# Optimization experiments

Hardware: AMD Instinct MI355X
Metric: run time of the kernel (lower is better)

The kernel has to match this reference:

```python
import jax, jax.numpy as jnp
import numpy as np

B, T = 128, 64
N_IN, H1, H2, N_OUT = 2048, 2048, 1024, 128
BETA = 0.95
THRESH = 1.0  # snn.Leaky default threshold


def spike(x):
    # Heaviside firing function (forward of snntorch ATan surrogate)
    return (x > 0).astype(x.dtype)


def setup_inputs() -> dict:
    key = jax.random.key(0)
    ks = jax.random.split(key, 5)

    def linear_params(k, fan_in, fan_out):
        k1, k2 = jax.random.split(k)
        bound = 1.0 / np.sqrt(fan_in)  # torch nn.Linear default init
        W = jax.random.uniform(k1, (fan_out, fan_in), minval=-bound, maxval=bound, dtype=jnp.float32)
        b = jax.random.uniform(k2, (fan_out,), minval=-bound, maxval=bound, dtype=jnp.float32)
        return W, b

    W0, b0 = linear_params(ks[0], N_IN, N_IN)
    W1, b1 = linear_params(ks[1], N_IN, H1)
    W2, b2 = linear_params(ks[2], H1, H2)
    W3, b3 = linear_params(ks[3], H2, N_OUT)
    x = jax.random.normal(ks[4], (B, T, N_IN), dtype=jnp.float32)
    return {"x": x, "W0": W0, "b0": b0, "W1": W1, "b1": b1,
            "W2": W2, "b2": b2, "W3": W3, "b3": b3}


def _lif(cur, mem):
    # snntorch Leaky (reset_mechanism='subtract'): reset computed from incoming mem
    reset = spike(mem - THRESH)
    mem_new = BETA * mem + cur - reset * THRESH
    spk = spike(mem_new - THRESH)
    return spk, mem_new


def reference(x, W0, b0, W1, b1, W2, b2, W3, b3):
    Bb = x.shape[0]
    dt = x.dtype
    mems0 = (jnp.zeros((Bb, N_IN), dt), jnp.zeros((Bb, H1), dt),
             jnp.zeros((Bb, H2), dt), jnp.zeros((Bb, N_OUT), dt))
    x_tbf = jnp.swapaxes(x, 0, 1)  # [T, B, N_IN]

    def step(carry, x_t):
        m0, m1, m2, m3 = carry
        s0, m0 = _lif(x_t @ W0.T + b0, m0)
        s1, m1 = _lif(s0 @ W1.T + b1, m1)
        s2, m2 = _lif(s1 @ W2.T + b2, m2)
        s3, m3 = _lif(s2 @ W3.T + b3, m3)
        return (m0, m1, m2, m3), (s3, m3)

    _, (spk3, mem3) = jax.lax.scan(step, mems0, x_tbf)
    # [T, B, N_OUT] -> [B, T, N_OUT]
    return jnp.swapaxes(spk3, 0, 1), jnp.swapaxes(mem3, 0, 1)
```

## Files before the change

kernel.cpp:

```cpp
#include <hip/hip_runtime.h>
#include <cstddef>
#include <cstdint>


#define BETA 0.95f

static constexpr int B_ = 128;
static constexpr int T_ = 64;
static constexpr int M_ = B_ * T_;
static constexpr int NOUT = 128;

typedef __bf16 bf16x8 __attribute__((ext_vector_type(8)));
typedef _Float16 f16x8 __attribute__((ext_vector_type(8)));
typedef float f32x4 __attribute__((ext_vector_type(4)));
typedef ushort u16x8 __attribute__((ext_vector_type(8)));

__device__ __forceinline__ ushort f32_bf16_rne(float f) {
  uint32_t u = __float_as_uint(f);
  uint32_t r = u + 0x7FFFu + ((u >> 16) & 1u);
  return (ushort)(r >> 16);
}
__device__ __forceinline__ float bf16_f32(ushort h) {
  return __uint_as_float(((uint32_t)h) << 16);
}
__device__ __forceinline__ ushort h2u(_Float16 h) {
  union { _Float16 h; ushort u; } v; v.h = h; return v.u;
}
__device__ __forceinline__ _Float16 u2h(ushort u) {
  union { ushort u; _Float16 h; } v; v.u = u; return v.h;
}

__global__ __launch_bounds__(256) void split2_f16(
    const float* __restrict__ S, ushort* __restrict__ oh,
    ushort* __restrict__ ol, int K, int nslots)
{
  int g = blockIdx.x * 256 + threadIdx.x;
  if (g >= nslots) return;
  int spr = K >> 3;
  int row = g / spr;
  int sl = g - row * spr;
  int kb = sl >> 3;
  int slot = sl & 7;
  int pslot = (slot & 4) | ((slot & 3) ^ ((row >> 1) & 3));
  const float* src = S + (size_t)row * K + (kb << 6) + (slot << 3);
  size_t dst = (size_t)row * K + (kb << 6) + (pslot << 3);
  u16x8 vh, vl;
#pragma unroll
  for (int i = 0; i < 8; ++i) {
    float f = src[i];
    _Float16 h = (_Float16)f;
    float hf = (float)h;
    if (fabsf(hf) < 6.103515625e-05f) { h = (_Float16)0.0f; hf = 0.0f; }
    float l = (f - hf) * 4096.0f;
    vh[i] = h2u(h);
    vl[i] = h2u((_Float16)l);
  }
  *reinterpret_cast<u16x8*>(oh + dst) = vh;
  *reinterpret_cast<u16x8*>(ol + dst) = vl;
}

__global__ __launch_bounds__(256) void split3_swz(
    const float* __restrict__ S, ushort* __restrict__ o1,
    ushort* __restrict__ o2, ushort* __restrict__ o3,
    int K, int nslots)
{
  int g = blockIdx.x * 256 + threadIdx.x;
  if (g >= nslots) return;
  int spr = K >> 3;
  int row = g / spr;
  int sl = g - row * spr;
  int kb = sl >> 3;
  int slot = sl & 7;
  int pslot = slot ^ (row & 7);
  const float* src = S + (size_t)row * K + (kb << 6) + (slot << 3);
  size_t dst = (size_t)row * K + (kb << 6) + (pslot << 3);
  u16x8 v1, v2, v3;
#pragma unroll
  for (int i = 0; i < 8; ++i) {
    float f = src[i];
    ushort h1 = f32_bf16_rne(f);
    float r = f - bf16_f32(h1);
    ushort h2 = f32_bf16_rne(r);
    float r2 = r - bf16_f32(h2);
    ushort h3 = f32_bf16_rne(r2);
    v1[i] = h1; v2[i] = h2; v3[i] = h3;
  }
  *reinterpret_cast<u16x8*>(o1 + dst) = v1;
  *reinterpret_cast<u16x8*>(o2 + dst) = v2;
  *reinterpret_cast<u16x8*>(o3 + dst) = v3;
}

__global__ __launch_bounds__(512) void gemm_corr(
    const ushort* __restrict__ A, const ushort* __restrict__ Bh,
    int NT, int K, int N, ushort* __restrict__ curC)
{
  __shared__ __align__(16) ushort lds[49152];

  const int tid = threadIdx.x;
  const int lane = tid & 63;
  const int wid = tid >> 6;
  const int wm = wid >> 1;
  const int wn = wid & 1;
  const int lane15 = lane & 15;
  const int lhi = lane >> 4;
  const int sg2 = lhi ^ ((lane15 >> 1) & 3);

  int nwg = gridDim.x * gridDim.y;
  int bid = blockIdx.y * gridDim.x + blockIdx.x;
  int cpx = nwg >> 3;
  int sw = (bid & 7) * cpx + (bid >> 3);
  int bx = sw % gridDim.x, by = sw / gridDim.x;
  const int bm = by * 256, bn = bx * 128;

  const int sr2 = tid >> 2;
  const int sg = tid & 3;

  auto stage = [&](int t1, int h, int d) {
    const int k0 = t1 * 64 + h * 32;
#pragma unroll
    for (int l = 0; l < 2; ++l) {
      int row = sr2 + l * 128;
      __builtin_amdgcn_global_load_lds(
          (const __attribute__((address_space(1))) void*)(A + (size_t)(bm + row) * K + k0 + sg * 8),
          (__attribute__((address_space(3))) void*)(lds + d * 16384 + h * 8192 + row * 32 + sg * 8),
          16, 0, 0);
    }
    __builtin_amdgcn_global_load_lds(
        (const __attribute__((address_space(1))) void*)(Bh + (size_t)(bn + sr2) * K + k0 + sg * 8),
        (__attribute__((address_space(3))) void*)(lds + 32768 + (d * 2 + h) * 4096 + sr2 * 32 + sg * 8),
        16, 0, 0);
  };

  f32x4 accC[4][4];
#pragma unroll
  for (int i = 0; i < 4; ++i)
#pragma unroll
    for (int j = 0; j < 4; ++j)
      accC[i][j] = (f32x4){0.f, 0.f, 0.f, 0.f};

  stage(0, 0, 0);
  stage(0, 1, 0);
  asm volatile("s_waitcnt vmcnt(3)" ::: "memory");
  asm volatile("s_barrier" ::: "memory");

  for (int t = 0; t < NT; ++t) {
    const int d = t & 1;
#pragma unroll
    for (int h = 0; h < 2; ++h) {
      f16x8 af[4];
      const ushort* Ab = lds + (d * 2 + h) * 8192;
#pragma unroll
      for (int i = 0; i < 4; ++i)
        af[i] = *(const f16x8*)(Ab + (wm * 64 + i * 16 + lane15) * 32 + sg2 * 8);

      if (t < NT - 1) {
        stage(t + 1, h, d ^ 1);
        asm volatile("s_waitcnt vmcnt(3)" ::: "memory");
      } else if (h == 0) {
        asm volatile("s_waitcnt vmcnt(0)" ::: "memory");
      }
      asm volatile("s_barrier" ::: "memory");

      const ushort* Bb = lds + 32768 + (d * 2 + h) * 4096;
      f16x8 bf[4];
#pragma unroll
      for (int j = 0; j < 4; ++j)
        bf[j] = *(const f16x8*)(Bb + (wn * 64 + j * 16 + lane15) * 32 + sg2 * 8);
      __builtin_amdgcn_s_setprio(1);
#pragma unroll
      for (int i = 0; i < 4; ++i)
#pragma unroll
        for (int j = 0; j < 4; ++j)
          accC[i][j] = __builtin_amdgcn_mfma_f32_16x16x32_f16(af[i], bf[j], accC[i][j], 0, 0, 0);
      __builtin_amdgcn_s_setprio(0);
      asm volatile("s_barrier" ::: "memory");
    }
  }

#pragma unroll
  for (int i = 0; i < 4; ++i) {
    int r0 = bm + wm * 64 + i * 16 + lhi * 4;
#pragma unroll
    for (int j = 0; j < 4; ++j) {
      int col = bn + wn * 64 + j * 16 + lane15;
      f32x4 vc = accC[i][j];
#pragma unroll
      for (int r = 0; r < 4; ++r)
        curC[(size_t)(r0 + r) * N + col] = h2u((_Float16)vc[r]);
    }
  }
}

template<int HASC, int FMT>
__global__ __launch_bounds__(512) void gemm_mainL(
    const ushort* __restrict__ A,
    const ushort* __restrict__ Bh, const ushort* __restrict__ Bl,
    int NT, int K, int N,
    const ushort* __restrict__ curCin,
    const float* __restrict__ bias, ushort* __restrict__ spk)
{
  __shared__ __align__(16) ushort lds[67584];

  const int tid = threadIdx.x;
  const int lane = tid & 63;
  const int wid = tid >> 6;
  const int wm = wid >> 1;
  const int wn = wid & 1;
  const int lane15 = lane & 15;
  const int lhi = lane >> 4;
  const int sg2 = lhi ^ ((lane15 >> 1) & 3);

  int nwg = gridDim.x * gridDim.y;
  int bid = blockIdx.y * gridDim.x + blockIdx.x;
  int cpx = nwg >> 3;
  int sw = (bid & 7) * cpx + (bid >> 3);
  int bx = sw % gridDim.x, by = sw / gridDim.x;
  const int bm = by * 256, bn = bx * 128;

  const int sr2 = tid >> 2;
  const int sg = tid & 3;

  auto stage = [&](int t1, int d) {
#pragma unroll
    for (int h = 0; h < 2; ++h) {
      const int k0 = t1 * 64 + h * 32;
#pragma unroll
      for (int l = 0; l < 2; ++l) {
        int row = sr2 + l * 128;
        __builtin_amdgcn_global_load_lds(
            (const __attribute__((address_space(1))) void*)(A + (size_t)(bm + row) * K + k0 + sg * 8),
            (__attribute__((address_space(3))) void*)(lds + d * 16384 + h * 8192 + row * 32 + sg * 8),
            16, 0, 0);
      }
#pragma unroll
      for (int s = 0; s < 2; ++s) {
        const ushort* Bp = (s == 0) ? Bh : Bl;
        __builtin_amdgcn_global_load_lds(
            (const __attribute__((address_space(1))) void*)(Bp + (size_t)(bn + sr2) * K + k0 + sg * 8),
            (__attribute__((address_space(3))) void*)(lds + 32768 + ((d * 2 + h) * 2 + s) * 4096 + sr2 * 32 + sg * 8),
            16, 0, 0);
      }
    }
  };

  f32x4 accM[4][4], accC[4][4];
#pragma unroll
  for (int i = 0; i < 4; ++i)
#pragma unroll
    for (int j = 0; j < 4; ++j) {
      accM[i][j] = (f32x4){0.f, 0.f, 0.f, 0.f};
      accC[i][j] = (f32x4){0.f, 0.f, 0.f, 0.f};
    }

  stage(0, 0);
  asm volatile("s_waitcnt vmcnt(0)" ::: "memory");
  asm volatile("s_barrier" ::: "memory");

  for (int t = 0; t < NT; ++t) {
    const int d = t & 1;
    const int tn = (t + 1 < NT) ? t + 1 : NT - 1;
    stage(tn, d ^ 1);
    asm volatile("s_waitcnt vmcnt(8)" ::: "memory");
    asm volatile("s_barrier" ::: "memory");

    __builtin_amdgcn_s_setprio(1);
#pragma unroll
    for (int h = 0; h < 2; ++h) {
      f16x8 af[4];
      const ushort* Ab = lds + (d * 2 + h) * 8192;
#pragma unroll
      for (int i = 0; i < 4; ++i)
        af[i] = *(const f16x8*)(Ab + (wm * 64 + i * 16 + lane15) * 32 + sg2 * 8);
#pragma unroll
      for (int s = 0; s < 2; ++s) {
        const ushort* Bb = lds + 32768 + ((d * 2 + h) * 2 + s) * 4096;
        f16x8 bf[4];
#pragma unroll
        for (int j = 0; j < 4; ++j)
          bf[j] = *(const f16x8*)(Bb + (wn * 64 + j * 16 + lane15) * 32 + sg2 * 8);
        if (s == 0) {
#pragma unroll
          for (int i = 0; i < 4; ++i)
#pragma unroll
            for (int j = 0; j < 4; ++j)
              accM[i][j] = __builtin_amdgcn_mfma_f32_16x16x32_f16(af[i], bf[j], accM[i][j], 0, 0, 0);
        } else {
#pragma unroll
          for (int i = 0; i < 4; ++i)
#pragma unroll
            for (int j = 0; j < 4; ++j)
              accC[i][j] = __builtin_amdgcn_mfma_f32_16x16x32_f16(af[i], bf[j], accC[i][j], 0, 0, 0);
        }
      }
    }
    __builtin_amdgcn_s_setprio(0);
    asm volatile("s_barrier" ::: "memory");
  }

  asm volatile("s_waitcnt vmcnt(0)" ::: "memory");
  __syncthreads();

  float* curb = (float*)lds;
#pragma unroll
  for (int i = 0; i < 4; ++i) {
    int rl = wm * 64 + i * 16 + lhi * 4;
#pragma unroll
    for (int j = 0; j < 4; ++j) {
      int cl = wn * 64 + j * 16 + lane15;
      f32x4 vm = accM[i][j], vc = accC[i][j];
#pragma unroll
      for (int r = 0; r < 4; ++r) {
        float corr = vc[r];
        if (HASC)
          corr += (float)u2h(curCin[(size_t)(bm + rl + r) * N + (bn + cl)]);
        curb[(rl + r) * 132 + cl] = __fmaf_rn(corr, 2.44140625e-4f, vm[r]);
      }
    }
  }
  __syncthreads();

  {
    int b2 = tid >> 7;
    int n = tid & 127;
    int cg = bn + n;
    float bv = bias[cg];
    int nb6 = cg >> 6;
    int sl = (cg >> 3) & 7;
    int nlow = cg & 7;
    const ushort one = FMT ? (ushort)0x3C00 : (ushort)0x3F80;
    float mem = 0.f;
    for (int t2 = 0; t2 < 64; ++t2) {
      float c = __fadd_rn(curb[(b2 * 64 + t2) * 132 + n], bv);
      float reset = ((mem - 1.0f) > 0.0f) ? 1.0f : 0.0f;
      mem = __fmul_rn(BETA, mem);
      mem = __fadd_rn(mem, c);
      mem = __fadd_rn(mem, -reset);
      ushort sv = ((mem - 1.0f) > 0.0f) ? one : (ushort)0;
      int m = bm + b2 * 64 + t2;
      int ps = FMT ? ((sl & 4) | ((sl & 3) ^ ((m >> 1) & 3)))
                   : (sl ^ (m & 7));
      spk[(size_t)m * N + (nb6 << 6) + (ps << 3) + nlow] = sv;
    }
  }
}

__global__ __launch_bounds__(256) void gemm_seg_lif(
    const ushort* __restrict__ A0,
    const ushort* __restrict__ B0, const ushort* __restrict__ B1,
    const ushort* __restrict__ B2,
    const float* __restrict__ bias,
    float* __restrict__ spk_out, float* __restrict__ mem_out)
{
  __shared__ ushort As[128 * 64];
  __shared__ ushort Bs[128 * 64];
  __shared__ float curb[128 * 132];

  const int tid = threadIdx.x;
  const int lane = tid & 63;
  const int wid = tid >> 6;
  const int wr = wid >> 1, wc = wid & 1;
  const int lane15 = lane & 15;
  const int lhi = lane >> 4;
  const int rswz = lane15 & 7;
  const int lrow = lane >> 3, lslot = lane & 7;

  int nwg = gridDim.x * gridDim.y;
  int bid = blockIdx.y * gridDim.x + blockIdx.x;
  int cpx = nwg >> 3;
  int sw = (bid & 7) * cpx + (bid >> 3);
  int bx = sw % gridDim.x, by = sw / gridDim.x;
  const int bm = by * 128, bn = bx * 128;

  f32x4 accM[4][4], accC[4][4];
#pragma unroll
  for (int i = 0; i < 4; ++i)
#pragma unroll
    for (int j = 0; j < 4; ++j) {
      accM[i][j] = (f32x4){0.f, 0.f, 0.f, 0.f};
      accC[i][j] = (f32x4){0.f, 0.f, 0.f, 0.f};
    }

  const bool isA = (wid < 2);
  ushort* lbase = isA ? As : Bs;
  const int rowbase0 = isA ? bm : bn;
  const int chunk0 = (wid & 1) * 8;

  for (int p = 0; p < 3; ++p) {
    const ushort* Bp = (p == 0) ? B0 : ((p == 1) ? B1 : B2);
    const ushort* gsrc = isA ? A0 : Bp;
    for (int k0 = 0; k0 < 1024; k0 += 64) {
      __syncthreads();
#pragma unroll
      for (int c = 0; c < 8; ++c) {
        int chunk = chunk0 + c;
        int row = chunk * 8 + lrow;
        const ushort* g = gsrc + (size_t)(rowbase0 + row) * 1024 + k0 + (lslot << 3);
        __builtin_amdgcn_global_load_lds(
            (const __attribute__((address_space(1))) void*)(g),
            (__attribute__((address_space(3))) void*)(lbase + chunk * 512),
            16, 0, 0);
      }
      __syncthreads();
#pragma unroll
      for (int kk = 0; kk < 2; ++kk) {
        int sp = ((kk << 2) | lhi) ^ rswz;
        bf16x8 af[4], bg[4];
#pragma unroll
        for (int i = 0; i < 4; ++i)
          af[i] = *(const bf16x8*)(As + (wr * 64 + i * 16 + lane15) * 64 + sp * 8);
#pragma unroll
        for (int j = 0; j < 4; ++j)
          bg[j] = *(const bf16x8*)(Bs + (wc * 64 + j * 16 + lane15) * 64 + sp * 8);
        if (p == 0) {
#pragma unroll
          for (int i = 0; i < 4; ++i)
#pragma unroll
            for (int j = 0; j < 4; ++j)
              accM[i][j] = __builtin_amdgcn_mfma_f32_16x16x32_bf16(af[i], bg[j], accM[i][j], 0, 0, 0);
        } else {
#pragma unroll
          for (int i = 0; i < 4; ++i)
#pragma unroll
            for (int j = 0; j < 4; ++j)
              accC[i][j] = __builtin_amdgcn_mfma_f32_16x16x32_bf16(af[i], bg[j], accC[i][j], 0, 0, 0);
        }
      }
    }
  }

  __syncthreads();
#pragma unroll
  for (int j = 0; j < 4; ++j) {
    int cl = wc * 64 + j * 16 + lane15;
#pragma unroll
    for (int i = 0; i < 4; ++i) {
      int rl = wr * 64 + i * 16 + lhi * 4;
      f32x4 vm = accM[i][j], vc = accC[i][j];
#pragma unroll
      for (int r = 0; r < 4; ++r)
        curb[(rl + r) * 132 + cl] = vm[r] + vc[r];
    }
  }
  __syncthreads();

  {
    int b2 = tid >> 7;
    int n = tid & 127;
    float bv = bias[bn + n];
    float mem = 0.f;
    for (int t2 = 0; t2 < 64; ++t2) {
      float c = __fadd_rn(curb[(b2 * 64 + t2) * 132 + n], bv);
      float reset = ((mem - 1.0f) > 0.0f) ? 1.0f : 0.0f;
      mem = __fmul_rn(BETA, mem);
      mem = __fadd_rn(mem, c);
      mem = __fadd_rn(mem, -reset);
      int m = bm + b2 * 64 + t2;
      size_t idx = (size_t)m * 128 + bn + n;
      spk_out[idx] = ((mem - 1.0f) > 0.0f) ? 1.0f : 0.0f;
      mem_out[idx] = mem;
    }
  }
}

extern "C" void kernel_launch(void* const* d_in, const int* in_sizes, int n_in,
                              void* d_out, int out_size, void* d_ws, size_t ws_size,
                              hipStream_t stream)
{
  const float* x  = (const float*)d_in[0];
  const float* W0 = (const float*)d_in[1];
  const float* b0 = (const float*)d_in[2];
  const float* W1 = (const float*)d_in[3];
  const float* b1 = (const float*)d_in[4];
  const float* W2 = (const float*)d_in[5];
  const float* b2 = (const float*)d_in[6];
  const float* W3 = (const float*)d_in[7];
  const float* b3 = (const float*)d_in[8];
  float* out = (float*)d_out;

  char* ws = (char*)d_ws;
  size_t off = 0;
  auto take = [&](size_t bytes) -> char* {
    char* p = ws + off;
    off += (bytes + 255) & ~(size_t)255;
    return p;
  };

  ushort* w0h = (ushort*)take((size_t)2048 * 2048 * 2);
  ushort* w0l = (ushort*)take((size_t)2048 * 2048 * 2);
  ushort* w1h = (ushort*)take((size_t)2048 * 2048 * 2);
  ushort* w1l = (ushort*)take((size_t)2048 * 2048 * 2);
  ushort* w2h = (ushort*)take((size_t)1024 * 2048 * 2);
  ushort* w2l = (ushort*)take((size_t)1024 * 2048 * 2);
  ushort* w3s[3];
  for (int i = 0; i < 3; ++i) w3s[i] = (ushort*)take((size_t)128 * 1024 * 2);
  ushort* xh = (ushort*)take((size_t)M_ * 2048 * 2);
  ushort* xl = (ushort*)take((size_t)M_ * 2048 * 2);
  ushort* s0 = (ushort*)take((size_t)M_ * 2048 * 2);
  ushort* curC = (ushort*)take((size_t)M_ * 2048 * 2);
  ushort* s1 = xh;
  ushort* s2 = xl;

  dim3 blk(256);
  dim3 fblk(512);

  {
    int ns = 2048 * 2048 / 8;
    split2_f16<<<(ns + 255) / 256, blk, 0, stream>>>(W0, w0h, w0l, 2048, ns);
    split2_f16<<<(ns + 255) / 256, blk, 0, stream>>>(W1, w1h, w1l, 2048, ns);
    ns = 1024 * 2048 / 8;
    split2_f16<<<(ns + 255) / 256, blk, 0, stream>>>(W2, w2h, w2l, 2048, ns);
    ns = 128 * 1024 / 8;
    split3_swz<<<(ns + 255) / 256, blk, 0, stream>>>(W3, w3s[0], w3s[1], w3s[2], 1024, ns);
    ns = M_ * 2048 / 8;
    split2_f16<<<(ns + 255) / 256, blk, 0, stream>>>(x, xh, xl, 2048, ns);
  }

  {
    dim3 grid(2048 / 128, M_ / 256);
    gemm_corr<<<grid, fblk, 0, stream>>>(xl, w0h, 32, 2048, 2048, curC);
    gemm_mainL<1, 1><<<grid, fblk, 0, stream>>>(xh, w0h, w0l, 32, 2048, 2048, curC, b0, s0);
  }
  {
    dim3 grid(2048 / 128, M_ / 256);
    gemm_mainL<0, 1><<<grid, fblk, 0, stream>>>(s0, w1h, w1l, 32, 2048, 2048, nullptr, b1, s1);
  }
  {
    dim3 grid(1024 / 128, M_ / 256);
    gemm_mainL<0, 0><<<grid, fblk, 0, stream>>>(s1, w2h, w2l, 32, 2048, 1024, nullptr, b2, s2);
  }
  {
    float* spk3 = out;
    float* mem3 = out + (size_t)M_ * NOUT;
    gemm_seg_lif<<<dim3(1, 64), blk, 0, stream>>>(s2, w3s[0], w3s[1], w3s[2], b3, spk3, mem3);
  }
}
```

Baseline: 535.8 us.

## Fuse layer-0 correction GEMM into main LIF GEMM with two-phase K loop

```diff
diff --git a/kernel.cpp b/kernel.cpp
--- a/kernel.cpp
+++ b/kernel.cpp
@@ -90,11 +90,15 @@
   *reinterpret_cast<u16x8*>(o3 + dst) = v3;
 }
 
-__global__ __launch_bounds__(512) void gemm_corr(
-    const ushort* __restrict__ A, const ushort* __restrict__ Bh,
-    int NT, int K, int N, ushort* __restrict__ curC)
+template<int NP, int FMT>
+__global__ __launch_bounds__(512) void gemm_mainL(
+    const ushort* __restrict__ A0p, const ushort* __restrict__ A1p,
+    const ushort* __restrict__ Bh0, const ushort* __restrict__ Bl0,
+    const ushort* __restrict__ Bh1, const ushort* __restrict__ Bl1,
+    int K, int N,
+    const float* __restrict__ bias, ushort* __restrict__ spk)
 {
-  __shared__ __align__(16) ushort lds[49152];
+  __shared__ __align__(16) ushort lds[67584];
 
   const int tid = threadIdx.x;
   const int lane = tid & 63;
@@ -115,36 +119,52 @@
   const int sr2 = tid >> 2;
   const int sg = tid & 3;
 
+  const ushort* Aps[2] = {A0p, (NP == 2) ? A1p : A0p};
+  const ushort* Bhs[2] = {Bh0, (NP == 2) ? Bh1 : Bh0};
+  const ushort* Bls[2] = {Bl0, (NP == 2) ? Bl1 : Bl0};
+
   auto stage = [&](int t1, int h, int d) {
-    const int k0 = t1 * 64 + h * 32;
+    const int pn = t1 >> 5;
+    const int k0 = (t1 & 31) * 64 + h * 32;
+    const ushort* Ap = Aps[pn];
 #pragma unroll
     for (int l = 0; l < 2; ++l) {
       int row = sr2 + l * 128;
       __builtin_amdgcn_global_load_lds(
-          (const __attribute__((address_space(1))) void*)(A + (size_t)(bm + row) * K + k0 + sg * 8),
+          (const __attribute__((address_space(1))) void*)(Ap + (size_t)(bm + row) * K + k0 + sg * 8),
           (__attribute__((address_space(3))) void*)(lds + d * 16384 + h * 8192 + row * 32 + sg * 8),
           16, 0, 0);
     }
-    __builtin_amdgcn_global_load_lds(
-        (const __attribute__((address_space(1))) void*)(Bh + (size_t)(bn + sr2) * K + k0 + sg * 8),
-        (__attribute__((address_space(3))) void*)(lds + 32768 + (d * 2 + h) * 4096 + sr2 * 32 + sg * 8),
-        16, 0, 0);
+#pragma unroll
+    for (int s = 0; s < 2; ++s) {
+      const ushort* Bp = (s == 0) ? Bhs[pn] : Bls[pn];
+      __builtin_amdgcn_global_load_lds(
+          (const __attribute__((address_space(1))) void*)(Bp + (size_t)(bn + sr2) * K + k0 + sg * 8),
+          (__attribute__((address_space(3))) void*)(lds + 32768 + ((d * 2 + h) * 2 + s) * 4096 + sr2 * 32 + sg * 8),
+          16, 0, 0);
+    }
   };
 
-  f32x4 accC[4][4];
+  f32x4 accM[4][4], accC[4][4];
 #pragma unroll
   for (int i = 0; i < 4; ++i)
 #pragma unroll
-    for (int j = 0; j < 4; ++j)
+    for (int j = 0; j < 4; ++j) {
+      accM[i][j] = (f32x4){0.f, 0.f, 0.f, 0.f};
       accC[i][j] = (f32x4){0.f, 0.f, 0.f, 0.f};
+    }
+
+  const int NT = NP * 32;
 
   stage(0, 0, 0);
   stage(0, 1, 0);
-  asm volatile("s_waitcnt vmcnt(3)" ::: "memory");
+  asm volatile("s_waitcnt vmcnt(0)" ::: "memory");
   asm volatile("s_barrier" ::: "memory");
 
   for (int t = 0; t < NT; ++t) {
     const int d = t & 1;
+    const int p = t >> 5;
+    const int nb = (NP == 2 && p == 1) ? 1 : 2;
 #pragma unroll
     for (int h = 0; h < 2; ++h) {
       f16x8 af[4];
@@ -155,146 +175,39 @@
 
       if (t < NT - 1) {
         stage(t + 1, h, d ^ 1);
-        asm volatile("s_waitcnt vmcnt(3)" ::: "memory");
+        asm volatile("s_waitcnt vmcnt(4)" ::: "memory");
       } else if (h == 0) {
         asm volatile("s_waitcnt vmcnt(0)" ::: "memory");
       }
       asm volatile("s_barrier" ::: "memory");
 
-      const ushort* Bb = lds + 32768 + (d * 2 + h) * 4096;
-      f16x8 bf[4];
-#pragma unroll
-      for (int j = 0; j < 4; ++j)
-        bf[j] = *(const f16x8*)(Bb + (wn * 64 + j * 16 + lane15) * 32 + sg2 * 8);
       __builtin_amdgcn_s_setprio(1);
 #pragma unroll
-      for (int i = 0; i < 4; ++i)
-#pragma unroll
-        for (int j = 0; j < 4; ++j)
-          accC[i][j] = __builtin_amdgcn_mfma_f32_16x16x32_f16(af[i], bf[j], accC[i][j], 0, 0, 0);
+      for (int s = 0; s < 2; ++s) {
+        if (s < nb) {
+          const ushort* Bb = lds + 32768 + ((d * 2 + h) * 2 + s) * 4096;
+          f16x8 bf[4];
+#pragma unroll
+          for (int j = 0; j < 4; ++j)
+            bf[j] = *(const f16x8*)(Bb + (wn * 64 + j * 16 + lane15) * 32 + sg2 * 8);
+          if (p == 0 && s == 0) {
+#pragma unroll
+            for (int i = 0; i < 4; ++i)
+#pragma unroll
+              for (int j = 0; j < 4; ++j)
+                accM[i][j] = __builtin_amdgcn_mfma_f32_16x16x32_f16(af[i], bf[j], accM[i][j], 0, 0, 0);
+          } else {
+#pragma unroll
+            for (int i = 0; i < 4; ++i)
+#pragma unroll
+              for (int j = 0; j < 4; ++j)
+                accC[i][j] = __builtin_amdgcn_mfma_f32_16x16x32_f16(af[i], bf[j], accC[i][j], 0, 0, 0);
+          }
+        }
+      }
       __builtin_amdgcn_s_setprio(0);
       asm volatile("s_barrier" ::: "memory");
     }
-  }
-
-#pragma unroll
-  for (int i = 0; i < 4; ++i) {
-    int r0 = bm + wm * 64 + i * 16 + lhi * 4;
-#pragma unroll
-    for (int j = 0; j < 4; ++j) {
-      int col = bn + wn * 64 + j * 16 + lane15;
-      f32x4 vc = accC[i][j];
-#pragma unroll
-      for (int r = 0; r < 4; ++r)
-        curC[(size_t)(r0 + r) * N + col] = h2u((_Float16)vc[r]);
-    }
-  }
-}
-
-template<int HASC, int FMT>
-__global__ __launch_bounds__(512) void gemm_mainL(
-    const ushort* __restrict__ A,
-    const ushort* __restrict__ Bh, const ushort* __restrict__ Bl,
-    int NT, int K, int N,
-    const ushort* __restrict__ curCin,
-    const float* __restrict__ bias, ushort* __restrict__ spk)
-{
-  __shared__ __align__(16) ushort lds[67584];
-
-  const int tid = threadIdx.x;
-  const int lane = tid & 63;
-  const int wid = tid >> 6;
-  const int wm = wid >> 1;
-  const int wn = wid & 1;
-  const int lane15 = lane & 15;
-  const int lhi = lane >> 4;
-  const int sg2 = lhi ^ ((lane15 >> 1) & 3);
-
-  int nwg = gridDim.x * gridDim.y;
-  int bid = blockIdx.y * gridDim.x + blockIdx.x;
-  int cpx = nwg >> 3;
-  int sw = (bid & 7) * cpx + (bid >> 3);
-  int bx = sw % gridDim.x, by = sw / gridDim.x;
-  const int bm = by * 256, bn = bx * 128;
-
-  const int sr2 = tid >> 2;
-  const int sg = tid & 3;
-
-  auto stage = [&](int t1, int d) {
-#pragma unroll
-    for (int h = 0; h < 2; ++h) {
-      const int k0 = t1 * 64 + h * 32;
-#pragma unroll
-      for (int l = 0; l < 2; ++l) {
-        int row = sr2 + l * 128;
-        __builtin_amdgcn_global_load_lds(
-            (const __attribute__((address_space(1))) void*)(A + (size_t)(bm + row) * K + k0 + sg * 8),
-            (__attribute__((address_space(3))) void*)(lds + d * 16384 + h * 8192 + row * 32 + sg * 8),
-            16, 0, 0);
-      }
-#pragma unroll
-      for (int s = 0; s < 2; ++s) {
-        const ushort* Bp = (s == 0) ? Bh : Bl;
-        __builtin_amdgcn_global_load_lds(
-            (const __attribute__((address_space(1))) void*)(Bp + (size_t)(bn + sr2) * K + k0 + sg * 8),
-            (__attribute__((address_space(3))) void*)(lds + 32768 + ((d * 2 + h) * 2 + s) * 4096 + sr2 * 32 + sg * 8),
-            16, 0, 0);
-      }
-    }
-  };
-
-  f32x4 accM[4][4], accC[4][4];
-#pragma unroll
-  for (int i = 0; i < 4; ++i)
-#pragma unroll
-    for (int j = 0; j < 4; ++j) {
-      accM[i][j] = (f32x4){0.f, 0.f, 0.f, 0.f};
-      accC[i][j] = (f32x4){0.f, 0.f, 0.f, 0.f};
-    }
-
-  stage(0, 0);
-  asm volatile("s_waitcnt vmcnt(0)" ::: "memory");
-  asm volatile("s_barrier" ::: "memory");
-
-  for (int t = 0; t < NT; ++t) {
-    const int d = t & 1;
-    const int tn = (t + 1 < NT) ? t + 1 : NT - 1;
-    stage(tn, d ^ 1);
-    asm volatile("s_waitcnt vmcnt(8)" ::: "memory");
-    asm volatile("s_barrier" ::: "memory");
-
-    __builtin_amdgcn_s_setprio(1);
-#pragma unroll
-    for (int h = 0; h < 2; ++h) {
-      f16x8 af[4];
-      const ushort* Ab = lds + (d * 2 + h) * 8192;
-#pragma unroll
-      for (int i = 0; i < 4; ++i)
-        af[i] = *(const f16x8*)(Ab + (wm * 64 + i * 16 + lane15) * 32 + sg2 * 8);
-#pragma unroll
-      for (int s = 0; s < 2; ++s) {
-        const ushort* Bb = lds + 32768 + ((d * 2 + h) * 2 + s) * 4096;
-        f16x8 bf[4];
-#pragma unroll
-        for (int j = 0; j < 4; ++j)
-          bf[j] = *(const f16x8*)(Bb + (wn * 64 + j * 16 + lane15) * 32 + sg2 * 8);
-        if (s == 0) {
-#pragma unroll
-          for (int i = 0; i < 4; ++i)
-#pragma unroll
-            for (int j = 0; j < 4; ++j)
-              accM[i][j] = __builtin_amdgcn_mfma_f32_16x16x32_f16(af[i], bf[j], accM[i][j], 0, 0, 0);
-        } else {
-#pragma unroll
-          for (int i = 0; i < 4; ++i)
-#pragma unroll
-            for (int j = 0; j < 4; ++j)
-              accC[i][j] = __builtin_amdgcn_mfma_f32_16x16x32_f16(af[i], bf[j], accC[i][j], 0, 0, 0);
-        }
-      }
-    }
-    __builtin_amdgcn_s_setprio(0);
-    asm volatile("s_barrier" ::: "memory");
   }
 
   asm volatile("s_waitcnt vmcnt(0)" ::: "memory");
@@ -309,12 +222,8 @@
       int cl = wn * 64 + j * 16 + lane15;
       f32x4 vm = accM[i][j], vc = accC[i][j];
 #pragma unroll
-      for (int r = 0; r < 4; ++r) {
-        float corr = vc[r];
-        if (HASC)
-          corr += (float)u2h(curCin[(size_t)(bm + rl + r) * N + (bn + cl)]);
-        curb[(rl + r) * 132 + cl] = __fmaf_rn(corr, 2.44140625e-4f, vm[r]);
-      }
+      for (int r = 0; r < 4; ++r)
+        curb[(rl + r) * 132 + cl] = __fmaf_rn(vc[r], 2.44140625e-4f, vm[r]);
     }
   }
   __syncthreads();
@@ -496,7 +405,6 @@
   ushort* xh = (ushort*)take((size_t)M_ * 2048 * 2);
   ushort* xl = (ushort*)take((size_t)M_ * 2048 * 2);
   ushort* s0 = (ushort*)take((size_t)M_ * 2048 * 2);
-  ushort* curC = (ushort*)take((size_t)M_ * 2048 * 2);
   ushort* s1 = xh;
   ushort* s2 = xl;
 
@@ -517,16 +425,18 @@
 
   {
     dim3 grid(2048 / 128, M_ / 256);
-    gemm_corr<<<grid, fblk, 0, stream>>>(xl, w0h, 32, 2048, 2048, curC);
-    gemm_mainL<1, 1><<<grid, fblk, 0, stream>>>(xh, w0h, w0l, 32, 2048, 2048, curC, b0, s0);
+    gemm_mainL<2, 1><<<grid, fblk, 0, stream>>>(
+        xh, xl, w0h, w0l, w0h, w0h, 2048, 2048, b0, s0);
   }
   {
     dim3 grid(2048 / 128, M_ / 256);
-    gemm_mainL<0, 1><<<grid, fblk, 0, stream>>>(s0, w1h, w1l, 32, 2048, 2048, nullptr, b1, s1);
+    gemm_mainL<1, 1><<<grid, fblk, 0, stream>>>(
+        s0, s0, w1h, w1l, w1h, w1l, 2048, 2048, b1, s1);
   }
   {
     dim3 grid(1024 / 128, M_ / 256);
-    gemm_mainL<0, 0><<<grid, fblk, 0, stream>>>(s1, w2h, w2l, 32, 2048, 1024, nullptr, b2, s2);
+    gemm_mainL<1, 0><<<grid, fblk, 0, stream>>>(
+        s1, s1, w2h, w2l, w2h, w2l, 2048, 1024, b2, s2);
   }
   {
     float* spk3 = out;
```

New measurement: 478.0 us, median of 3. -10.8%, faster.
